# Performance work log

Measured on AMD Instinct MI355X. Metric: run time of the kernel, lower is better.

The kernel has to match this reference:

```python
import jax, jax.numpy as jnp
import numpy as np

N = 100000   # nodes
E = 1600000  # edges
G = 1024     # graphs
V = 51       # attr_dims[0]+1 embedding rows (padding_idx=0)
EMB = 32
H = 2        # heads
D = 64       # hidden_dim (per-head out channels)
DC = H * D   # 128 = dim_conv
NEG_GAT = 0.2   # PyG GATConv default negative_slope
NEG_ACT = 0.05  # module's leaky_relu slope
LN_EPS = 1e-5


def setup_inputs() -> dict:
    key = jax.random.key(0)
    ks = jax.random.split(key, 20)
    def nrm(k, shape, scale=0.1):
        return jax.random.normal(k, shape, dtype=jnp.float32) * scale
    x = jax.random.randint(ks[0], (N, 1), 0, V)
    edge_index = jax.random.randint(ks[1], (2, E), 0, N)
    batch_idx = jnp.sort(jax.random.randint(ks[2], (N,), 0, G))
    return {
        'x': x, 'edge_index': edge_index, 'batch_idx': batch_idx,
        'emb': nrm(ks[3], (V, EMB)).at[0].set(0.0),  # padding_idx=0
        'ln_g': jnp.ones((EMB,), jnp.float32), 'ln_b': jnp.zeros((EMB,), jnp.float32),
        'W1': nrm(ks[4], (EMB, DC)), 'a_src1': nrm(ks[5], (H, D)), 'a_dst1': nrm(ks[6], (H, D)), 'b1': nrm(ks[7], (DC,)),
        'W2': nrm(ks[8], (DC, DC)), 'a_src2': nrm(ks[9], (H, D)), 'a_dst2': nrm(ks[10], (H, D)), 'b2': nrm(ks[11], (DC,)),
        'gw1': nrm(ks[12], (DC, D)), 'gb1': nrm(ks[13], (D,)),
        'gw2': nrm(ks[14], (D, 1)), 'gb2': nrm(ks[15], (1,)),
    }


def _gat_conv(xf, src, dst, W, a_src, a_dst, b):
    # xf: [N, in]; returns [N, H*D]. PyG GATConv, eval mode (attn dropout off).
    xw = (xf @ W).reshape(N, H, D)                           # [N,H,D]
    al_s = jnp.einsum('nhd,hd->nh', xw, a_src)
    al_d = jnp.einsum('nhd,hd->nh', xw, a_dst)
    e = jax.nn.leaky_relu(al_s[src] + al_d[dst], NEG_GAT)    # [E',H]
    m = jax.ops.segment_max(e, dst, num_segments=N)
    ex = jnp.exp(e - m[dst])
    s = jax.ops.segment_sum(ex, dst, num_segments=N)
    alpha = ex / s[dst]                                      # segment softmax over incoming edges
    msg = xw[src] * alpha[:, :, None]                        # [E',H,D]
    out = jax.ops.segment_sum(msg, dst, num_segments=N)      # [N,H,D]
    return out.reshape(N, DC) + b


def reference(x, edge_index, batch_idx, emb, ln_g, ln_b,
              W1, a_src1, a_dst1, b1, W2, a_src2, a_dst2, b2,
              gw1, gb1, gw2, gb2):
    # embedding + LayerNorm (dropout off in eval)
    xe = emb[x[:, 0]]                                        # [N,32]
    mu = jnp.mean(xe, axis=-1, keepdims=True)
    var = jnp.var(xe, axis=-1, keepdims=True)
    xe = (xe - mu) * jax.lax.rsqrt(var + LN_EPS) * ln_g + ln_b
    # add self loops (GATConv add_self_loops=True)
    ar = jnp.arange(N, dtype=edge_index.dtype)
    src = jnp.concatenate([edge_index[0], ar])
    dst = jnp.concatenate([edge_index[1], ar])
    h = jax.nn.leaky_relu(_gat_conv(xe, src, dst, W1, a_src1, a_dst1, b1), NEG_ACT)
    h = _gat_conv(h, src, dst, W2, a_src2, a_dst2, b2)       # [N,128]
    # attentional aggregation over graphs
    gate = jax.nn.leaky_relu(h @ gw1 + gb1, NEG_ACT) @ gw2 + gb2   # [N,1]
    gm = jax.ops.segment_max(gate, batch_idx, num_segments=G)
    ge = jnp.exp(gate - gm[batch_idx])
    gs = jax.ops.segment_sum(ge, batch_idx, num_segments=G)
    w = ge / gs[batch_idx]
    z = jax.ops.segment_sum(w * h, batch_idx, num_segments=G)      # [G,128]
    return h, z
```

## Files before the change

### kernel.cpp

```cpp
#include <hip/hip_runtime.h>
#include <hip/hip_bf16.h>
#include <stdint.h>

typedef unsigned short u16;
typedef unsigned int   u32;
typedef __attribute__((ext_vector_type(8))) short bf16x8;
typedef __attribute__((ext_vector_type(4))) float f32x4;

#define NEG_GAT 0.2f
#define NEG_ACT 0.05f
#define LN_EPS  1e-5f
#define NPARAM  15

__device__ __forceinline__ float bf2f(u32 bits16){
  union { u32 u; float f; } v; v.u = bits16 << 16; return v.f;
}
__device__ __forceinline__ u16 f2bf(float f){
  union { float f; u32 u; } v; v.f = f;
  u32 u = v.u;
  u32 r = (u + 0x7fffu + ((u >> 16) & 1u)) >> 16;
  return (u16)r;
}
__device__ __forceinline__ float lrelu(float x, float s){ return fmaxf(x, s * x); }

__device__ __forceinline__ int geti(const int* __restrict__ p, int i, int enc){
  return p[enc ? (2 * i) : i];
}


struct CvtParams {
  const void* src[NPARAM];
  float*      dst[NPARAM];
  int         n[NPARAM];
};

#define MAXB  2048

__global__ void k_detect(const u32* __restrict__ ln_g_raw, const int* __restrict__ ei_raw,
                         int* __restrict__ flags, int* __restrict__ bcnt)
{
  const int t = threadIdx.x;
  for (int i = t; i < MAXB; i += 256) bcnt[i] = 0;
  if (t == 0){
    flags[0] = (ln_g_raw[0] == 0x3F800000u) ? 0 : 1;
    int zeros = 0;
    for (int j = 0; j < 64; j++) if (ei_raw[2 * j + 1] == 0) zeros++;
    flags[1] = (zeros >= 60) ? 1 : 0;
    flags[2] = 0;
    flags[3] = 0;
  }
}

__global__ void k_convert(CvtParams P, const int* __restrict__ flag)
{
  const int pi  = blockIdx.y;
  const int idx = blockIdx.x * 256 + threadIdx.x;
  if (idx >= P.n[pi]) return;
  if (*flag == 0) P.dst[pi][idx] = ((const float*)P.src[pi])[idx];
  else            P.dst[pi][idx] = bf2f(((const u16*)P.src[pi])[idx]);
}


__global__ void k_checks(const int* __restrict__ batch, const int* __restrict__ x,
                         const int* __restrict__ iflag,
                         int n, int V, int* __restrict__ errflag)
{
  int i = blockIdx.x * 256 + threadIdx.x;
  const int enc = *iflag;
  if (i < n){
    int v = geti(x, i, enc);
    if ((unsigned)v >= (unsigned)V) atomicOr(errflag, 16);
    if (i < n - 1 && geti(batch, i, enc) > geti(batch, i + 1, enc)) atomicOr(errflag, 8);
  }
}

__global__ void k_check_edges(const int* __restrict__ ei, const int* __restrict__ iflag,
                              int E, int n, int* __restrict__ errflag)
{
  int e = blockIdx.x * 256 + threadIdx.x;
  if (e < E){
    int enc = *iflag;
    int s = geti(ei, e, enc);
    int d = geti(ei, E + e, enc);
    if ((unsigned)s >= (unsigned)n || (unsigned)d >= (unsigned)n) atomicOr(errflag, 32);
  }
}


__global__ void k_hist(const int* __restrict__ ei, const int* __restrict__ iflag,
                       int* __restrict__ counts, int E, int n)
{
  int e = blockIdx.x * 256 + threadIdx.x;
  if (e < E){
    int d = geti(ei, E + e, *iflag);
    d = min(max(d, 0), n - 1);
    atomicAdd(&counts[d], 1);
  }
}

__global__ void k_scanA(const int* __restrict__ counts, int* __restrict__ rowptr,
                        int* __restrict__ bsums, int n)
{
  __shared__ int sd[1024];
  int tid = threadIdx.x;
  int gid = blockIdx.x * 1024 + tid;
  int v = (gid < n) ? counts[gid] : 0;
  sd[tid] = v;
  __syncthreads();
  for (int off = 1; off < 1024; off <<= 1){
    int t = 0;
    if (tid >= off) t = sd[tid - off];
    __syncthreads();
    if (tid >= off) sd[tid] += t;
    __syncthreads();
  }
  if (gid < n) rowptr[gid] = sd[tid] - v;
  if (tid == 1023) bsums[blockIdx.x] = sd[1023];
}

__global__ void k_scanB(const int* __restrict__ bsums, int* __restrict__ boffs, int nb)
{
  __shared__ int sd[128];
  int tid = threadIdx.x;
  int v = (tid < nb) ? bsums[tid] : 0;
  sd[tid] = v;
  __syncthreads();
  for (int off = 1; off < 128; off <<= 1){
    int t = 0;
    if (tid >= off) t = sd[tid - off];
    __syncthreads();
    if (tid >= off) sd[tid] += t;
    __syncthreads();
  }
  if (tid < nb) boffs[tid] = sd[tid] - v;
}

__global__ void k_scanC(int* __restrict__ rowptr, const int* __restrict__ boffs,
                        int* __restrict__ cursor, int n, int Etot)
{
  int gid = blockIdx.x * 1024 + threadIdx.x;
  if (gid < n){
    int v = rowptr[gid] + boffs[blockIdx.x];
    rowptr[gid] = v;
    cursor[gid] = v;
  }
  if (gid == 0) rowptr[n] = Etot;
}

__global__ void k_scatter(const int* __restrict__ ei, const int* __restrict__ iflag,
                          int* __restrict__ cursor, int* __restrict__ csr, int E, int n)
{
  int e = blockIdx.x * 256 + threadIdx.x;
  if (e < E){
    int enc = *iflag;
    int s = geti(ei, e, enc);
    int d = geti(ei, E + e, enc);
    d = min(max(d, 0), n - 1);
    int pos = atomicAdd(&cursor[d], 1);
    csr[pos] = s;
  }
}

__global__ void k_check_rows(const int* __restrict__ rowptr, const int* __restrict__ cursor,
                             int n, int* __restrict__ errflag)
{
  int i = blockIdx.x * 256 + threadIdx.x;
  if (i < n){
    if (cursor[i] != rowptr[i + 1]) atomicOr(errflag, 1);
    if (i == 0 && rowptr[0] != 0)   atomicOr(errflag, 4);
  }
}

__global__ void k_check_csr(const int* __restrict__ csr, int E, int n, int* __restrict__ errflag)
{
  int e = blockIdx.x * 256 + threadIdx.x;
  if (e < E && (unsigned)csr[e] >= (unsigned)n) atomicOr(errflag, 2);
}


#define BSH   9
#define BSZ   512
#define BMSK  511
#define BINB  8192
#define BTH   512

__global__ void k_bhist(const int* __restrict__ ei, const int* __restrict__ iflag,
                        int* __restrict__ bcnt, int E, int N, int nbuck)
{
  __shared__ int h[MAXB];
  const int t = threadIdx.x;
  for (int i = t; i < nbuck; i += 256) h[i] = 0;
  __syncthreads();
  const int enc = *iflag;
  for (int e = blockIdx.x * 256 + t; e < E; e += gridDim.x * 256){
    int d = geti(ei, E + e, enc);
    d = min(max(d, 0), N - 1);
    atomicAdd(&h[d >> BSH], 1);
  }
  __syncthreads();
  for (int i = t; i < nbuck; i += 256){
    int c = h[i];
    if (c) atomicAdd(&bcnt[i], c);
  }
}

__global__ void k_bscan(const int* __restrict__ bcnt, int* __restrict__ boff,
                        int* __restrict__ gcur, int* __restrict__ rowptr,
                        int nbuck, int N, int E)
{
  __shared__ int sd[MAXB];
  const int lane = threadIdx.x;
  for (int i = lane; i < nbuck; i += 64) sd[i] = bcnt[i];
  __syncthreads();
  const int L = (nbuck + 63) >> 6;
  const int b0 = lane * L;
  int sum = 0;
  for (int j = 0; j < L; j++){ int idx = b0 + j; if (idx < nbuck) sum += sd[idx]; }
  int excl = sum;
  for (int off = 1; off < 64; off <<= 1){
    int x = __shfl_up(excl, off);
    if (lane >= off) excl += x;
  }
  excl -= sum;
  int run = excl;
  for (int j = 0; j < L; j++){
    int idx = b0 + j;
    if (idx < nbuck){ boff[idx] = run; gcur[idx] = run; run += sd[idx]; }
  }
  if (lane == 0){ boff[nbuck] = E; rowptr[N] = E; }
}

__global__ __launch_bounds__(BTH) void k_bbin(
    const int* __restrict__ ei, const int* __restrict__ iflag,
    int* __restrict__ gcur, u32* __restrict__ binned,
    int E, int N, int nbuck, int* __restrict__ errflag)
{
  __shared__ u32 stage[BINB];
  __shared__ u16 sbk[BINB];
  __shared__ int hist[MAXB];
  __shared__ int base[MAXB];
  __shared__ int gpos[MAXB];
  const int t   = threadIdx.x;
  const int e0  = blockIdx.x * BINB;
  const int cnt = min(BINB, E - e0);
  const int enc = *iflag;

  for (int i = t; i < nbuck; i += BTH) hist[i] = 0;
  __syncthreads();

  u32 pv[16]; int bk[16]; int rk[16];
  int bad = 0;
  #pragma unroll
  for (int k = 0; k < 16; k++){
    bk[k] = -1;
    int lo = k * BTH + t;
    if (lo < cnt){
      int e = e0 + lo;
      int s = geti(ei, e, enc);
      int d = geti(ei, E + e, enc);
      if ((unsigned)s >= (unsigned)N || (unsigned)d >= (unsigned)N) bad = 1;
      s = min(max(s, 0), N - 1);
      d = min(max(d, 0), N - 1);
      int b = d >> BSH;
      pv[k] = ((u32)s << BSH) | (u32)(d & BMSK);
      bk[k] = b;
      rk[k] = atomicAdd(&hist[b], 1);
    }
  }
  if (bad) atomicOr(errflag, 32);
  __syncthreads();

  if (t < 64){
    const int L = (nbuck + 63) >> 6;
    const int b0 = t * L;
    int sum = 0;
    for (int j = 0; j < L; j++){ int idx = b0 + j; if (idx < nbuck) sum += hist[idx]; }
    int excl = sum;
    for (int off = 1; off < 64; off <<= 1){
      int x = __shfl_up(excl, off);
      if (t >= off) excl += x;
    }
    excl -= sum;
    int run = excl;
    for (int j = 0; j < L; j++){
      int idx = b0 + j;
      if (idx < nbuck){ base[idx] = run; run += hist[idx]; }
    }
  }
  __syncthreads();

  for (int i = t; i < nbuck; i += BTH){
    int c = hist[i];
    gpos[i] = c ? atomicAdd(&gcur[i], c) : 0;
  }
  __syncthreads();

  #pragma unroll
  for (int k = 0; k < 16; k++){
    if (bk[k] >= 0){
      int slot = base[bk[k]] + rk[k];
      stage[slot] = pv[k];
      sbk[slot]   = (u16)bk[k];
    }
  }
  __syncthreads();

  for (int j = t; j < cnt; j += BTH){
    int b = sbk[j];
    binned[gpos[b] + (j - base[b])] = stage[j];
  }
}

__global__ __launch_bounds__(256) void k_bcsr(
    const u32* __restrict__ binned, const int* __restrict__ boff,
    int* __restrict__ rowptr, int* __restrict__ csr, int N, int nbuck)
{
  __shared__ int cnt[BSZ];
  __shared__ int rp[BSZ];
  __shared__ int cur[BSZ];
  const int b = blockIdx.x;
  const int t = threadIdx.x;
  const int lo = boff[b], hi = boff[b + 1];

  for (int i = t; i < BSZ; i += 256){ cnt[i] = 0; cur[i] = 0; }
  __syncthreads();

  for (int j = lo + t; j < hi; j += 256)
    atomicAdd(&cnt[binned[j] & BMSK], 1);
  __syncthreads();

  if (t < 64){
    const int b0 = t * 8;
    int sum = 0;
    #pragma unroll
    for (int j = 0; j < 8; j++) sum += cnt[b0 + j];
    int excl = sum;
    for (int off = 1; off < 64; off <<= 1){
      int x = __shfl_up(excl, off);
      if (t >= off) excl += x;
    }
    excl -= sum;
    int run = excl;
    #pragma unroll
    for (int j = 0; j < 8; j++){ rp[b0 + j] = run; run += cnt[b0 + j]; }
  }
  __syncthreads();

  const int node0 = b << BSH;
  for (int i = t; i < BSZ; i += 256){
    int node = node0 + i;
    if (node < N) rowptr[node] = lo + rp[i];
  }

  for (int j = lo + t; j < hi; j += 256){
    u32 pvv = binned[j];
    int dl  = pvv & BMSK;
    int pos = lo + rp[dl] + atomicAdd(&cur[dl], 1);
    csr[pos] = (int)(pvv >> BSH);
  }
}


__global__ void k_stamp_if(const int* __restrict__ errflag, float* __restrict__ out, int nel)
{
  int f = *errflag;
  if (f == 0) return;
  float s = 500.0f + 100.0f * (float)f;
  for (int i = blockIdx.x * 256 + threadIdx.x; i < nel; i += gridDim.x * 256) out[i] = s;
}

__global__ void k_stamp(float* __restrict__ out, int nel, float val)
{
  for (int i = blockIdx.x * 256 + threadIdx.x; i < nel; i += gridDim.x * 256) out[i] = val;
}


__global__ __launch_bounds__(128) void k_tables(
    const float* __restrict__ emb,
    const float* __restrict__ ln_g, const float* __restrict__ ln_b,
    const float* __restrict__ W1, const float* __restrict__ a_src,
    const float* __restrict__ a_dst,
    const float* __restrict__ W2, const float* __restrict__ gw1,
    int V,
    u16* __restrict__ xwv, float* __restrict__ alsv, float* __restrict__ aldv,
    u16* __restrict__ pb2, u16* __restrict__ pbg)
{
  const int bid = blockIdx.x;
  const int t   = threadIdx.x;

  if (bid >= V){
    if (t >= 64) return;
    int pw = bid - V;
    const float* W; int ncols, ntiles, blk; u16* pb;
    if (pw < 32){ W = W2; ncols = 128; ntiles = 8; blk = pw;      pb = pb2; }
    else        { W = gw1; ncols = 64;  ntiles = 4; blk = pw - 32; pb = pbg; }
    const int ktile = blk / ntiles;
    const int ntile = blk % ntiles;
    const int n  = ntile * 16 + (t & 15);
    const int k0 = ktile * 32 + (t >> 4) * 8;
    u16* dst = pb + ((size_t)blk * 64 + t) * 8;
    #pragma unroll
    for (int j = 0; j < 8; j++)
      dst[j] = f2bf(W[(k0 + j) * ncols + n]);
    return;
  }

  __shared__ float se[32];
  __shared__ float stats[2];
  __shared__ float sxw[128];
  const int v = bid;
  if (t < 32) se[t] = emb[v * 32 + t];
  __syncthreads();
  if (t == 0){
    float s1 = 0.f, s2 = 0.f;
    for (int k = 0; k < 32; k++){ s1 += se[k]; s2 += se[k] * se[k]; }
    float mu = s1 * (1.f / 32.f);
    float var = s2 * (1.f / 32.f) - mu * mu;
    stats[0] = mu; stats[1] = rsqrtf(var + LN_EPS);
  }
  __syncthreads();
  const float mu = stats[0], rs = stats[1];
  float o = 0.f;
  for (int k = 0; k < 32; k++){
    float xe = (se[k] - mu) * rs * ln_g[k] + ln_b[k];
    o += xe * W1[k * 128 + t];
  }
  sxw[t] = o;
  xwv[v * 128 + t] = f2bf(o);
  __syncthreads();
  if (t < 2){
    float ps = 0.f, pd = 0.f;
    for (int d = 0; d < 64; d++){
      float vv = sxw[t * 64 + d];
      ps += vv * a_src[t * 64 + d];
      pd += vv * a_dst[t * 64 + d];
    }
    alsv[2 * v + t] = ps;
    aldv[2 * v + t] = pd;
  }
}


__global__ __launch_bounds__(256, 4) void k_gatw1(
    const int* __restrict__ rowptr, const int* __restrict__ csr,
    const int* __restrict__ x, const int* __restrict__ iflag,
    const float* __restrict__ alsv, const float* __restrict__ aldv,
    const u16* __restrict__ xwv, const float* __restrict__ bias,
    int N, int V, u16* __restrict__ out)
{
  extern __shared__ char smem[];
  float4* sedge = (float4*)smem;
  u16*    sxwv  = (u16*)(smem + 4096);
  float*  ET    = (float*)(smem + 4096 + (size_t)V * 256);

  const int tid = threadIdx.x;
  const int enc = *iflag;

  {
    const uint4* gx = (const uint4*)xwv;
    uint4* lx = (uint4*)sxwv;
    for (int idx = tid; idx < V * 16; idx += 256) lx[idx] = gx[idx];
  }
  {
    const int tot = V * V;
    for (int idx = tid; idx < tot; idx += 256){
      int vi = idx / V, v = idx - vi * V;
      ET[idx * 2]     = lrelu(alsv[2 * v]     + aldv[2 * vi],     NEG_GAT);
      ET[idx * 2 + 1] = lrelu(alsv[2 * v + 1] + aldv[2 * vi + 1], NEG_GAT);
    }
  }
  __syncthreads();
  {
    for (int r = tid; r < V * 2; r += 256){
      int vi = r >> 1, h = r & 1;
      float m = -3.0e38f;
      for (int v = 0; v < V; v++) m = fmaxf(m, ET[(vi * V + v) * 2 + h]);
      for (int v = 0; v < V; v++){
        int idx = (vi * V + v) * 2 + h;
        ET[idx] = __expf(ET[idx] - m);
      }
    }
  }
  __syncthreads();

  const int wave = tid >> 6;
  const int lane = tid & 63;
  const int sub  = lane >> 4;
  const int c16  = lane & 15;
  float4* mst = sedge + wave * 64;

  for (int i = blockIdx.x * 4 + wave; i < N; i += gridDim.x * 4){
    const int r0 = rowptr[i], deg = rowptr[i + 1] - r0, total = deg + 1;
    int vi = geti(x, i, enc); vi = min(max(vi, 0), V - 1);
    const float* ETrow = ET + (size_t)vi * V * 2;

    float sum0 = 0.f, sum1 = 0.f;
    float acc[8];
    #pragma unroll
    for (int r = 0; r < 8; r++) acc[r] = 0.f;

    for (int base = 0; base < total; base += 64){
      int k = base + lane;
      int vs = vi; float w0 = 0.f, w1 = 0.f;
      if (k < total){
        int s = (k < deg) ? csr[r0 + k] : i;
        int v = geti(x, s, enc);
        vs = min(max(v, 0), V - 1);
        float2 wv = *(const float2*)(ETrow + vs * 2);
        w0 = wv.x; w1 = wv.y;
      }
      sum0 += w0; sum1 += w1;
      mst[lane] = make_float4(__int_as_float(vs), w0, w1, 0.f);
      int cnt = min(64, total - base);
      int qmax = (cnt + 3) & ~3;
      for (int q = 0; q < qmax; q += 4){
        float4 md = mst[q + sub];
        int   vj = __float_as_int(md.x);
        float ej = (c16 < 8) ? md.y : md.z;
        uint4 w = *(const uint4*)(sxwv + vj * 128 + c16 * 8);
        acc[0] += ej * bf2f(w.x & 0xffffu); acc[1] += ej * bf2f(w.x >> 16);
        acc[2] += ej * bf2f(w.y & 0xffffu); acc[3] += ej * bf2f(w.y >> 16);
        acc[4] += ej * bf2f(w.z & 0xffffu); acc[5] += ej * bf2f(w.z >> 16);
        acc[6] += ej * bf2f(w.w & 0xffffu); acc[7] += ej * bf2f(w.w >> 16);
      }
    }

    #pragma unroll
    for (int off = 32; off; off >>= 1){
      sum0 += __shfl_xor(sum0, off);
      sum1 += __shfl_xor(sum1, off);
    }
    #pragma unroll
    for (int r = 0; r < 8; r++){
      acc[r] += __shfl_xor(acc[r], 16);
      acc[r] += __shfl_xor(acc[r], 32);
    }

    if (sub == 0){
      float inv = 1.f / ((c16 < 8) ? sum0 : sum1);
      const float4* bp = (const float4*)(bias + c16 * 8);
      float4 b0 = bp[0], b1 = bp[1];
      float o[8];
      o[0] = lrelu(acc[0] * inv + b0.x, NEG_ACT); o[1] = lrelu(acc[1] * inv + b0.y, NEG_ACT);
      o[2] = lrelu(acc[2] * inv + b0.z, NEG_ACT); o[3] = lrelu(acc[3] * inv + b0.w, NEG_ACT);
      o[4] = lrelu(acc[4] * inv + b1.x, NEG_ACT); o[5] = lrelu(acc[5] * inv + b1.y, NEG_ACT);
      o[6] = lrelu(acc[6] * inv + b1.z, NEG_ACT); o[7] = lrelu(acc[7] * inv + b1.w, NEG_ACT);
      uint4 pk;
      pk.x = (u32)f2bf(o[0]) | ((u32)f2bf(o[1]) << 16);
      pk.y = (u32)f2bf(o[2]) | ((u32)f2bf(o[3]) << 16);
      pk.z = (u32)f2bf(o[4]) | ((u32)f2bf(o[5]) << 16);
      pk.w = (u32)f2bf(o[6]) | ((u32)f2bf(o[7]) << 16);
      *(uint4*)(out + (size_t)i * 128 + c16 * 8) = pk;
    }
  }
}

__global__ __launch_bounds__(64, 8) void k_gatw1g(
    const int* __restrict__ rowptr, const int* __restrict__ csr,
    const int* __restrict__ x, const int* __restrict__ iflag,
    const float* __restrict__ alsv, const float* __restrict__ aldv,
    const u16* __restrict__ xwv, const float* __restrict__ bias,
    int V, u16* __restrict__ out)
{
  const int i    = blockIdx.x;
  const int lane = threadIdx.x;
  const int sub  = lane >> 4;
  const int c16  = lane & 15;
  const int enc  = *iflag;
  const int r0 = rowptr[i], deg = rowptr[i + 1] - r0, total = deg + 1;
  int vi = geti(x, i, enc); vi = min(max(vi, 0), V - 1);
  const float ad0 = aldv[2 * vi], ad1 = aldv[2 * vi + 1];

  float sum0 = 0.f, sum1 = 0.f;
  float acc[8];
  #pragma unroll
  for (int r = 0; r < 8; r++) acc[r] = 0.f;

  float m0 = -3.0e38f, m1 = -3.0e38f;
  for (int k = lane; k < total; k += 64){
    int s = (k < deg) ? csr[r0 + k] : i;
    int v = geti(x, s, enc); v = min(max(v, 0), V - 1);
    float2 as = *(const float2*)(alsv + 2 * v);
    m0 = fmaxf(m0, lrelu(as.x + ad0, NEG_GAT));
    m1 = fmaxf(m1, lrelu(as.y + ad1, NEG_GAT));
  }
  #pragma unroll
  for (int off = 32; off; off >>= 1){
    m0 = fmaxf(m0, __shfl_xor(m0, off));
    m1 = fmaxf(m1, __shfl_xor(m1, off));
  }
  for (int base = 0; base < total; base += 64){
    int k = base + lane;
    int vs = vi; float ex0 = 0.f, ex1 = 0.f;
    if (k < total){
      int s = (k < deg) ? csr[r0 + k] : i;
      int v = geti(x, s, enc); vs = min(max(v, 0), V - 1);
      float2 as = *(const float2*)(alsv + 2 * vs);
      ex0 = __expf(lrelu(as.x + ad0, NEG_GAT) - m0);
      ex1 = __expf(lrelu(as.y + ad1, NEG_GAT) - m1);
    }
    sum0 += ex0; sum1 += ex1;
    int cnt = min(64, total - base);
    int qmax = (cnt + 3) & ~3;
    for (int q = 0; q < qmax; q += 4){
      int   j  = q + sub;
      int   vj = __shfl(vs, j);
      float e0 = __shfl(ex0, j);
      float e1 = __shfl(ex1, j);
      float ej = (c16 < 8) ? e0 : e1;
      uint4 w = *(const uint4*)(xwv + (size_t)vj * 128 + c16 * 8);
      acc[0] += ej * bf2f(w.x & 0xffffu); acc[1] += ej * bf2f(w.x >> 16);
      acc[2] += ej * bf2f(w.y & 0xffffu); acc[3] += ej * bf2f(w.y >> 16);
      acc[4] += ej * bf2f(w.z & 0xffffu); acc[5] += ej * bf2f(w.z >> 16);
      acc[6] += ej * bf2f(w.w & 0xffffu); acc[7] += ej * bf2f(w.w >> 16);
    }
  }

  #pragma unroll
  for (int off = 32; off; off >>= 1){
    sum0 += __shfl_xor(sum0, off);
    sum1 += __shfl_xor(sum1, off);
  }
  #pragma unroll
  for (int r = 0; r < 8; r++){
    acc[r] += __shfl_xor(acc[r], 16);
    acc[r] += __shfl_xor(acc[r], 32);
  }

  if (sub == 0){
    float inv = 1.f / ((c16 < 8) ? sum0 : sum1);
    const float4* bp = (const float4*)(bias + c16 * 8);
    float4 b0 = bp[0], b1 = bp[1];
    float o[8];
    o[0] = lrelu(acc[0] * inv + b0.x, NEG_ACT); o[1] = lrelu(acc[1] * inv + b0.y, NEG_ACT);
    o[2] = lrelu(acc[2] * inv + b0.z, NEG_ACT); o[3] = lrelu(acc[3] * inv + b0.w, NEG_ACT);
    o[4] = lrelu(acc[4] * inv + b1.x, NEG_ACT); o[5] = lrelu(acc[5] * inv + b1.y, NEG_ACT);
    o[6] = lrelu(acc[6] * inv + b1.z, NEG_ACT); o[7] = lrelu(acc[7] * inv + b1.w, NEG_ACT);
    uint4 pk;
    pk.x = (u32)f2bf(o[0]) | ((u32)f2bf(o[1]) << 16);
    pk.y = (u32)f2bf(o[2]) | ((u32)f2bf(o[3]) << 16);
    pk.z = (u32)f2bf(o[4]) | ((u32)f2bf(o[5]) << 16);
    pk.w = (u32)f2bf(o[6]) | ((u32)f2bf(o[7]) << 16);
    *(uint4*)(out + (size_t)i * 128 + c16 * 8) = pk;
  }
}


__global__ __launch_bounds__(64, 8) void k_gatw2(
    const int* __restrict__ rowptr, const int* __restrict__ csr,
    const float* __restrict__ al_s, const float* __restrict__ al_d,
    const u16* __restrict__ xw, const float* __restrict__ bias,
    int apply_act, float* __restrict__ out)
{
  const int i    = blockIdx.x;
  const int lane = threadIdx.x;
  const int sub  = lane >> 4;
  const int c16  = lane & 15;
  const int r0 = rowptr[i], deg = rowptr[i + 1] - r0, total = deg + 1;
  const float2 ad = *(const float2*)(al_d + 2 * i);

  float sum0 = 0.f, sum1 = 0.f;
  float acc[8];
  #pragma unroll
  for (int r = 0; r < 8; r++) acc[r] = 0.f;

  if (total <= 64){
    int s = i;
    float a0 = -3.0e38f, a1 = -3.0e38f;
    if (lane < total){
      s = (lane < deg) ? csr[r0 + lane] : i;
      float2 as = *(const float2*)(al_s + 2 * s);
      a0 = lrelu(as.x + ad.x, NEG_GAT);
      a1 = lrelu(as.y + ad.y, NEG_GAT);
    }
    float m0 = a0, m1 = a1;
    #pragma unroll
    for (int off = 32; off; off >>= 1){
      m0 = fmaxf(m0, __shfl_xor(m0, off));
      m1 = fmaxf(m1, __shfl_xor(m1, off));
    }
    float ex0 = 0.f, ex1 = 0.f;
    if (lane < total){ ex0 = __expf(a0 - m0); ex1 = __expf(a1 - m1); }
    sum0 = ex0; sum1 = ex1;
    int qmax = (total + 3) & ~3;
    for (int q = 0; q < qmax; q += 4){
      int   j  = q + sub;
      int   sj = __shfl(s, j);
      float e0 = __shfl(ex0, j);
      float e1 = __shfl(ex1, j);
      float ej = (c16 < 8) ? e0 : e1;
      uint4 w = *(const uint4*)(xw + (size_t)sj * 128 + c16 * 8);
      acc[0] += ej * bf2f(w.x & 0xffffu); acc[1] += ej * bf2f(w.x >> 16);
      acc[2] += ej * bf2f(w.y & 0xffffu); acc[3] += ej * bf2f(w.y >> 16);
      acc[4] += ej * bf2f(w.z & 0xffffu); acc[5] += ej * bf2f(w.z >> 16);
      acc[6] += ej * bf2f(w.w & 0xffffu); acc[7] += ej * bf2f(w.w >> 16);
    }
  } else {
    float m0 = -3.0e38f, m1 = -3.0e38f;
    for (int k = lane; k < total; k += 64){
      int s = (k < deg) ? csr[r0 + k] : i;
      float2 as = *(const float2*)(al_s + 2 * s);
      m0 = fmaxf(m0, lrelu(as.x + ad.x, NEG_GAT));
      m1 = fmaxf(m1, lrelu(as.y + ad.y, NEG_GAT));
    }
    #pragma unroll
    for (int off = 32; off; off >>= 1){
      m0 = fmaxf(m0, __shfl_xor(m0, off));
      m1 = fmaxf(m1, __shfl_xor(m1, off));
    }
    for (int base = 0; base < total; base += 64){
      int k = base + lane;
      int s = i; float ex0 = 0.f, ex1 = 0.f;
      if (k < total){
        s = (k < deg) ? csr[r0 + k] : i;
        float2 as = *(const float2*)(al_s + 2 * s);
        ex0 = __expf(lrelu(as.x + ad.x, NEG_GAT) - m0);
        ex1 = __expf(lrelu(as.y + ad.y, NEG_GAT) - m1);
      }
      sum0 += ex0; sum1 += ex1;
      int cnt = min(64, total - base);
      int qmax = (cnt + 3) & ~3;
      for (int q = 0; q < qmax; q += 4){
        int   j  = q + sub;
        int   sj = __shfl(s, j);
        float e0 = __shfl(ex0, j);
        float e1 = __shfl(ex1, j);
        float ej = (c16 < 8) ? e0 : e1;
        uint4 w = *(const uint4*)(xw + (size_t)sj * 128 + c16 * 8);
        acc[0] += ej * bf2f(w.x & 0xffffu); acc[1] += ej * bf2f(w.x >> 16);
        acc[2] += ej * bf2f(w.y & 0xffffu); acc[3] += ej * bf2f(w.y >> 16);
        acc[4] += ej * bf2f(w.z & 0xffffu); acc[5] += ej * bf2f(w.z >> 16);
        acc[6] += ej * bf2f(w.w & 0xffffu); acc[7] += ej * bf2f(w.w >> 16);
      }
    }
  }

  #pragma unroll
  for (int off = 32; off; off >>= 1){
    sum0 += __shfl_xor(sum0, off);
    sum1 += __shfl_xor(sum1, off);
  }
  #pragma unroll
  for (int r = 0; r < 8; r++){
    acc[r] += __shfl_xor(acc[r], 16);
    acc[r] += __shfl_xor(acc[r], 32);
  }

  if (sub == 0){
    float inv = 1.f / ((c16 < 8) ? sum0 : sum1);
    const float4* bp = (const float4*)(bias + c16 * 8);
    float4 b0 = bp[0], b1 = bp[1];
    float4 o0, o1;
    o0.x = acc[0] * inv + b0.x; o0.y = acc[1] * inv + b0.y;
    o0.z = acc[2] * inv + b0.z; o0.w = acc[3] * inv + b0.w;
    o1.x = acc[4] * inv + b1.x; o1.y = acc[5] * inv + b1.y;
    o1.z = acc[6] * inv + b1.z; o1.w = acc[7] * inv + b1.w;
    if (apply_act){
      o0.x = lrelu(o0.x, NEG_ACT); o0.y = lrelu(o0.y, NEG_ACT);
      o0.z = lrelu(o0.z, NEG_ACT); o0.w = lrelu(o0.w, NEG_ACT);
      o1.x = lrelu(o1.x, NEG_ACT); o1.y = lrelu(o1.y, NEG_ACT);
      o1.z = lrelu(o1.z, NEG_ACT); o1.w = lrelu(o1.w, NEG_ACT);
    }
    float* op = out + (size_t)i * 128 + c16 * 8;
    *(float4*)op       = o0;
    *(float4*)(op + 4) = o1;
  }
}


__global__ __launch_bounds__(256, 2) void k_node2m(
    const u16* __restrict__ h1b, const u16* __restrict__ pb2,
    const float* __restrict__ a_src, const float* __restrict__ a_dst,
    int N, u16* __restrict__ xw, float* __restrict__ al_s, float* __restrict__ al_d)
{
  const int wave = threadIdx.x >> 6;
  const int lane = threadIdx.x & 63;
  const int rowbase = blockIdx.x * 64 + wave * 16;
  const int m    = lane & 15;
  const int quad = lane >> 4;

  int arow = rowbase + m; if (arow >= N) arow = N - 1;
  const u16* aptr = h1b + (size_t)arow * 128 + quad * 8;

  f32x4 acc[8];
  #pragma unroll
  for (int nt = 0; nt < 8; nt++) acc[nt] = (f32x4){0.f, 0.f, 0.f, 0.f};

  #pragma unroll
  for (int kt = 0; kt < 4; kt++){
    bf16x8 af = *(const bf16x8*)(aptr + kt * 32);
    const u16* bbase = pb2 + (((size_t)kt * 8) * 64 + lane) * 8;
    #pragma unroll
    for (int nt = 0; nt < 8; nt++){
      bf16x8 bf = *(const bf16x8*)(bbase + (size_t)nt * 64 * 8);
      acc[nt] = __builtin_amdgcn_mfma_f32_16x16x32_bf16(af, bf, acc[nt], 0, 0, 0);
    }
  }

  float asv[8], adv[8];
  #pragma unroll
  for (int nt = 0; nt < 8; nt++){
    asv[nt] = a_src[nt * 16 + m];
    adv[nt] = a_dst[nt * 16 + m];
  }
  #pragma unroll
  for (int r = 0; r < 4; r++){
    int row = rowbase + quad * 4 + r;
    bool ok = row < N;
    float s0 = 0.f, s1 = 0.f, d0 = 0.f, d1 = 0.f;
    #pragma unroll
    for (int nt = 0; nt < 8; nt++){
      float v = acc[nt][r];
      if (ok) xw[(size_t)row * 128 + nt * 16 + m] = f2bf(v);
      if (nt < 4){ s0 += v * asv[nt]; d0 += v * adv[nt]; }
      else       { s1 += v * asv[nt]; d1 += v * adv[nt]; }
    }
    #pragma unroll
    for (int off = 1; off < 16; off <<= 1){
      s0 += __shfl_xor(s0, off); s1 += __shfl_xor(s1, off);
      d0 += __shfl_xor(d0, off); d1 += __shfl_xor(d1, off);
    }
    if (ok && m == 0){
      al_s[2 * row] = s0; al_s[2 * row + 1] = s1;
      al_d[2 * row] = d0; al_d[2 * row + 1] = d1;
    }
  }
}


__global__ __launch_bounds__(256, 2) void k_gatem(
    const float* __restrict__ h, const u16* __restrict__ pbg,
    const float* __restrict__ gb1, const float* __restrict__ gw2,
    const float* __restrict__ gb2, int N, float* __restrict__ gate)
{
  const int wave = threadIdx.x >> 6;
  const int lane = threadIdx.x & 63;
  const int rowbase = blockIdx.x * 64 + wave * 16;
  const int m    = lane & 15;
  const int quad = lane >> 4;

  int arow = rowbase + m; if (arow >= N) arow = N - 1;
  const float* aptr = h + (size_t)arow * 128 + quad * 8;

  f32x4 acc[4];
  #pragma unroll
  for (int nt = 0; nt < 4; nt++) acc[nt] = (f32x4){0.f, 0.f, 0.f, 0.f};

  #pragma unroll
  for (int kt = 0; kt < 4; kt++){
    float4 a0 = *(const float4*)(aptr + kt * 32);
    float4 a1 = *(const float4*)(aptr + kt * 32 + 4);
    bf16x8 af;
    af[0] = (short)f2bf(a0.x); af[1] = (short)f2bf(a0.y);
    af[2] = (short)f2bf(a0.z); af[3] = (short)f2bf(a0.w);
    af[4] = (short)f2bf(a1.x); af[5] = (short)f2bf(a1.y);
    af[6] = (short)f2bf(a1.z); af[7] = (short)f2bf(a1.w);
    const u16* bbase = pbg + (((size_t)kt * 4) * 64 + lane) * 8;
    #pragma unroll
    for (int nt = 0; nt < 4; nt++){
      bf16x8 bf = *(const bf16x8*)(bbase + (size_t)nt * 64 * 8);
      acc[nt] = __builtin_amdgcn_mfma_f32_16x16x32_bf16(af, bf, acc[nt], 0, 0, 0);
    }
  }

  float gbv[4], g2v[4];
  #pragma unroll
  for (int nt = 0; nt < 4; nt++){
    gbv[nt] = gb1[nt * 16 + m];
    g2v[nt] = gw2[nt * 16 + m];
  }
  const float g2b = gb2[0];
  #pragma unroll
  for (int r = 0; r < 4; r++){
    int row = rowbase + quad * 4 + r;
    float q = 0.f;
    #pragma unroll
    for (int nt = 0; nt < 4; nt++)
      q += lrelu(acc[nt][r] + gbv[nt], NEG_ACT) * g2v[nt];
    #pragma unroll
    for (int off = 1; off < 16; off <<= 1) q += __shfl_xor(q, off);
    if (row < N && m == 0) gate[row] = q + g2b;
  }
}


__global__ __launch_bounds__(512) void k_graphsw(
    const int* __restrict__ batch, const int* __restrict__ iflag,
    const float* __restrict__ gate,
    const float* __restrict__ h, float* __restrict__ zout, int N)
{
  __shared__ int   range[2];
  __shared__ float red[16];
  __shared__ float sz[3][128];
  const int g = blockIdx.x, t = threadIdx.x;
  const int wave = t >> 6, lane = t & 63;
  if (t == 0){
    const int enc = *iflag;
    int lo = 0, hi = N;
    while (lo < hi){ int mid = (lo + hi) >> 1; if (geti(batch, mid, enc) < g) lo = mid + 1; else hi = mid; }
    range[0] = lo;
    hi = N;
    while (lo < hi){ int mid = (lo + hi) >> 1; if (geti(batch, mid, enc) < g + 1) lo = mid + 1; else hi = mid; }
    range[1] = lo;
  }
  __syncthreads();
  const int st = range[0], en = range[1];

  float m = -3.0e38f;
  for (int k = st + t; k < en; k += 512) m = fmaxf(m, gate[k]);
  #pragma unroll
  for (int off = 32; off; off >>= 1) m = fmaxf(m, __shfl_xor(m, off));
  if (lane == 0) red[wave] = m;
  __syncthreads();
  m = red[0];
  #pragma unroll
  for (int w = 1; w < 8; w++) m = fmaxf(m, red[w]);

  float s = 0.f;
  for (int k = st + t; k < en; k += 512) s += __expf(gate[k] - m);
  #pragma unroll
  for (int off = 32; off; off >>= 1) s += __shfl_xor(s, off);
  if (lane == 0) red[8 + wave] = s;
  __syncthreads();
  s = red[8];
  #pragma unroll
  for (int w = 9; w < 16; w++) s += red[w];

  const float inv = 1.f / s;
  const int quarter = t >> 7, t2 = t & 127;
  float z = 0.f;
  for (int k = st + quarter; k < en; k += 4){
    float wk = __expf(gate[k] - m) * inv;
    z += wk * h[(size_t)k * 128 + t2];
  }
  if (quarter) sz[quarter - 1][t2] = z;
  __syncthreads();
  if (quarter == 0) zout[(size_t)g * 128 + t2] = z + sz[0][t2] + sz[1][t2] + sz[2][t2];
}


extern "C" void kernel_launch(void* const* d_in, const int* in_sizes, int n_in,
                              void* d_out, int out_size, void* d_ws, size_t ws_size,
                              hipStream_t stream)
{
  const int* x      = (const int*)d_in[0];
  const int* ei     = (const int*)d_in[1];
  const int* batch  = (const int*)d_in[2];

  const int N = in_sizes[0];
  const int E = in_sizes[1] / 2;
  const int V = in_sizes[3] / 32;
  const int G = out_size / 128 - N;

  char* p = (char*)d_ws;
  auto alloc = [&](size_t bytes) -> char* {
    char* r = p; p += (bytes + 255) & ~(size_t)255; return r;
  };
  int*   multi  = (int*)  alloc((size_t)N * 4);
  int*   rowptr = (int*)  alloc((size_t)(N + 1) * 4);
  int*   csr    = (int*)  alloc((size_t)E * 4);
  int*   bsums  = (int*)  alloc(4096);
  int*   boffs  = (int*)  alloc(4096);
  int*   flags  = (int*)  alloc(256);
  int*   fflag  = flags;
  int*   iflag  = flags + 1;
  int*   errflg = flags + 2;
  float* al_s   = (float*)alloc((size_t)N * 2 * 4);
  float* al_d   = (float*)alloc((size_t)N * 2 * 4);
  u16*   xw     = (u16*)  alloc((size_t)N * 128 * 2);
  u16*   h1b    = (u16*)  alloc((size_t)N * 128 * 2);
  u16*   xwv    = (u16*)  alloc((size_t)V * 128 * 2);
  float* alsv   = (float*)alloc((size_t)V * 2 * 4);
  float* aldv   = (float*)alloc((size_t)V * 2 * 4);
  u16*   pb2    = (u16*)  alloc((size_t)128 * 128 * 2);
  u16*   pbg    = (u16*)  alloc((size_t)128 * 64 * 2);

  const int nbuck = (N + BSZ - 1) >> BSH;
  int*   bcnt   = (int*)  alloc((size_t)(MAXB) * 4);
  int*   boff   = (int*)  alloc((size_t)(MAXB + 1) * 4);
  int*   gcur   = (int*)  alloc((size_t)(MAXB) * 4);
  u32*   binned = (u32*)  alloc((size_t)E * 4);

  CvtParams cp;
  float* fpar[NPARAM];
  int maxn = 0;
  for (int pi = 0; pi < NPARAM; pi++){
    int n = in_sizes[3 + pi];
    fpar[pi] = (float*)alloc((size_t)n * 4);
    cp.src[pi] = d_in[3 + pi];
    cp.dst[pi] = fpar[pi];
    cp.n[pi]   = n;
    if (n > maxn) maxn = n;
  }
  const size_t needed = (size_t)(p - (char*)d_ws);

  const float* emb    = fpar[0];
  const float* ln_g   = fpar[1];
  const float* ln_b   = fpar[2];
  const float* W1     = fpar[3];
  const float* a_src1 = fpar[4];
  const float* a_dst1 = fpar[5];
  const float* b1     = fpar[6];
  const float* W2     = fpar[7];
  const float* a_src2 = fpar[8];
  const float* a_dst2 = fpar[9];
  const float* b2     = fpar[10];
  const float* gw1    = fpar[11];
  const float* gb1    = fpar[12];
  const float* gw2    = fpar[13];
  const float* gb2    = fpar[14];
  (void)n_in;

  if (ws_size < needed){
    k_stamp<<<512, 256, 0, stream>>>((float*)d_out, out_size, 9999.0f);
    return;
  }

  int*   counts = multi;
  int*   cursor = multi;
  float* gate   = (float*)multi;
  float* hbuf   = (float*)d_out;
  float* zbuf   = (float*)d_out + (size_t)N * 128;

  k_detect<<<1, 256, 0, stream>>>((const u32*)d_in[4], ei, flags, bcnt);
  dim3 cgrid((maxn + 255) / 256, NPARAM);
  k_convert<<<cgrid, 256, 0, stream>>>(cp, fflag);

  int eb = (E + 255) / 256;
  int nb = (N + 1023) / 1024;
  int nb256 = (N + 255) / 256;

  k_checks<<<nb256, 256, 0, stream>>>(batch, x, iflag, N, V, errflg);

  if (nbuck <= MAXB){
    k_bhist<<<256, 256, 0, stream>>>(ei, iflag, bcnt, E, N, nbuck);
    k_bscan<<<1, 64, 0, stream>>>(bcnt, boff, gcur, rowptr, nbuck, N, E);
    k_bbin<<<(E + BINB - 1) / BINB, BTH, 0, stream>>>(ei, iflag, gcur, binned, E, N, nbuck, errflg);
    k_bcsr<<<nbuck, 256, 0, stream>>>(binned, boff, rowptr, csr, N, nbuck);
  } else {
    k_check_edges<<<eb, 256, 0, stream>>>(ei, iflag, E, N, errflg);
    hipMemsetAsync(counts, 0, (size_t)N * 4, stream);
    hipMemsetAsync(csr, 0xFF, (size_t)E * 4, stream);
    k_hist<<<eb, 256, 0, stream>>>(ei, iflag, counts, E, N);
    k_scanA<<<nb, 1024, 0, stream>>>(counts, rowptr, bsums, N);
    k_scanB<<<1, 128, 0, stream>>>(bsums, boffs, nb);
    k_scanC<<<nb, 1024, 0, stream>>>(rowptr, boffs, cursor, N, E);
    k_scatter<<<eb, 256, 0, stream>>>(ei, iflag, cursor, csr, E, N);
    k_check_rows<<<nb256, 256, 0, stream>>>(rowptr, cursor, N, errflg);
    k_check_csr<<<eb, 256, 0, stream>>>(csr, E, N, errflg);
  }

  k_tables<<<V + 48, 128, 0, stream>>>(emb, ln_g, ln_b, W1, a_src1, a_dst1,
                                       W2, gw1, V, xwv, alsv, aldv, pb2, pbg);

  const size_t smem1 = 4096 + (size_t)V * 256 + (size_t)V * V * 8;
  if (V <= 64 && smem1 <= 64 * 1024){
    const int gwb = min(1024, (N + 3) / 4);
    k_gatw1<<<gwb, 256, smem1, stream>>>(rowptr, csr, x, iflag, alsv, aldv, xwv, b1, N, V, h1b);
  } else {
    k_gatw1g<<<N, 64, 0, stream>>>(rowptr, csr, x, iflag, alsv, aldv, xwv, b1, V, h1b);
  }

  const int gblk = (N + 63) / 64;
  k_node2m<<<gblk, 256, 0, stream>>>(h1b, pb2, a_src2, a_dst2, N, xw, al_s, al_d);

  k_gatw2<<<N, 64, 0, stream>>>(rowptr, csr, al_s, al_d, xw, b2, 0, hbuf);

  k_gatem<<<gblk, 256, 0, stream>>>(hbuf, pbg, gb1, gw2, gb2, N, gate);
  k_graphsw<<<G, 512, 0, stream>>>(batch, iflag, gate, hbuf, zbuf, N);

  k_stamp_if<<<512, 256, 0, stream>>>(errflg, (float*)d_out, out_size);
}
```

Baseline: 353.2 us.

## Fuse gate MLP into graph pooling kernel and fold input checks into CSR build

Removes the separate MFMA gate kernel and computes the gate scores inside the per-graph pooling kernel with an fp32 scalar dot product against gw1 held in shared memory. Each block handles one graph, so the rows of h it reads for the gate are read again right after for pooling. The x and batch validity checks move from their own kernel into k_bcsr, which cuts two launches. In exchange, the gate matmul drops from tensor-core MFMA to scalar FMA over LDS, and each block's 32KB+ of shared memory may limit occupancy.

```diff
diff --git a/kernel.cpp b/kernel.cpp
--- a/kernel.cpp
+++ b/kernel.cpp
@@ -313,7 +313,10 @@
 
 __global__ __launch_bounds__(256) void k_bcsr(
     const u32* __restrict__ binned, const int* __restrict__ boff,
-    int* __restrict__ rowptr, int* __restrict__ csr, int N, int nbuck)
+    const int* __restrict__ x, const int* __restrict__ batch,
+    const int* __restrict__ iflag, int V,
+    int* __restrict__ rowptr, int* __restrict__ csr, int N, int nbuck,
+    int* __restrict__ errflag)
 {
   __shared__ int cnt[BSZ];
   __shared__ int rp[BSZ];
@@ -321,8 +324,20 @@
   const int b = blockIdx.x;
   const int t = threadIdx.x;
   const int lo = boff[b], hi = boff[b + 1];
+  const int enc = *iflag;
+  const int node0 = b << BSH;
 
   for (int i = t; i < BSZ; i += 256){ cnt[i] = 0; cur[i] = 0; }
+
+  for (int i = t; i < BSZ; i += 256){
+    int node = node0 + i;
+    if (node < N){
+      int v = geti(x, node, enc);
+      if ((unsigned)v >= (unsigned)V) atomicOr(errflag, 16);
+      if (node < N - 1 && geti(batch, node, enc) > geti(batch, node + 1, enc))
+        atomicOr(errflag, 8);
+    }
+  }
   __syncthreads();
 
   for (int j = lo + t; j < hi; j += 256)
@@ -336,8 +351,8 @@
     for (int j = 0; j < 8; j++) sum += cnt[b0 + j];
     int excl = sum;
     for (int off = 1; off < 64; off <<= 1){
-      int x = __shfl_up(excl, off);
-      if (t >= off) excl += x;
+      int xq = __shfl_up(excl, off);
+      if (t >= off) excl += xq;
     }
     excl -= sum;
     int run = excl;
@@ -346,7 +361,6 @@
   }
   __syncthreads();
 
-  const int node0 = b << BSH;
   for (int i = t; i < BSZ; i += 256){
     int node = node0 + i;
     if (node < N) rowptr[node] = lo + rp[i];
@@ -380,28 +394,25 @@
     const float* __restrict__ ln_g, const float* __restrict__ ln_b,
     const float* __restrict__ W1, const float* __restrict__ a_src,
     const float* __restrict__ a_dst,
-    const float* __restrict__ W2, const float* __restrict__ gw1,
+    const float* __restrict__ W2,
     int V,
     u16* __restrict__ xwv, float* __restrict__ alsv, float* __restrict__ aldv,
-    u16* __restrict__ pb2, u16* __restrict__ pbg)
+    u16* __restrict__ pb2)
 {
   const int bid = blockIdx.x;
   const int t   = threadIdx.x;
 
   if (bid >= V){
     if (t >= 64) return;
-    int pw = bid - V;
-    const float* W; int ncols, ntiles, blk; u16* pb;
-    if (pw < 32){ W = W2; ncols = 128; ntiles = 8; blk = pw;      pb = pb2; }
-    else        { W = gw1; ncols = 64;  ntiles = 4; blk = pw - 32; pb = pbg; }
-    const int ktile = blk / ntiles;
-    const int ntile = blk % ntiles;
+    int blk = bid - V;
+    const int ktile = blk / 8;
+    const int ntile = blk % 8;
     const int n  = ntile * 16 + (t & 15);
     const int k0 = ktile * 32 + (t >> 4) * 8;
-    u16* dst = pb + ((size_t)blk * 64 + t) * 8;
+    u16* dst = pb2 + ((size_t)blk * 64 + t) * 8;
     #pragma unroll
     for (int j = 0; j < 8; j++)
-      dst[j] = f2bf(W[(k0 + j) * ncols + n]);
+      dst[j] = f2bf(W2[(k0 + j) * 128 + n]);
     return;
   }
 
@@ -828,70 +839,18 @@
 }
 
 
-__global__ __launch_bounds__(256, 2) void k_gatem(
-    const float* __restrict__ h, const u16* __restrict__ pbg,
-    const float* __restrict__ gb1, const float* __restrict__ gw2,
-    const float* __restrict__ gb2, int N, float* __restrict__ gate)
-{
-  const int wave = threadIdx.x >> 6;
-  const int lane = threadIdx.x & 63;
-  const int rowbase = blockIdx.x * 64 + wave * 16;
-  const int m    = lane & 15;
-  const int quad = lane >> 4;
-
-  int arow = rowbase + m; if (arow >= N) arow = N - 1;
-  const float* aptr = h + (size_t)arow * 128 + quad * 8;
-
-  f32x4 acc[4];
-  #pragma unroll
-  for (int nt = 0; nt < 4; nt++) acc[nt] = (f32x4){0.f, 0.f, 0.f, 0.f};
-
-  #pragma unroll
-  for (int kt = 0; kt < 4; kt++){
-    float4 a0 = *(const float4*)(aptr + kt * 32);
-    float4 a1 = *(const float4*)(aptr + kt * 32 + 4);
-    bf16x8 af;
-    af[0] = (short)f2bf(a0.x); af[1] = (short)f2bf(a0.y);
-    af[2] = (short)f2bf(a0.z); af[3] = (short)f2bf(a0.w);
-    af[4] = (short)f2bf(a1.x); af[5] = (short)f2bf(a1.y);
-    af[6] = (short)f2bf(a1.z); af[7] = (short)f2bf(a1.w);
-    const u16* bbase = pbg + (((size_t)kt * 4) * 64 + lane) * 8;
-    #pragma unroll
-    for (int nt = 0; nt < 4; nt++){
-      bf16x8 bf = *(const bf16x8*)(bbase + (size_t)nt * 64 * 8);
-      acc[nt] = __builtin_amdgcn_mfma_f32_16x16x32_bf16(af, bf, acc[nt], 0, 0, 0);
-    }
-  }
-
-  float gbv[4], g2v[4];
-  #pragma unroll
-  for (int nt = 0; nt < 4; nt++){
-    gbv[nt] = gb1[nt * 16 + m];
-    g2v[nt] = gw2[nt * 16 + m];
-  }
-  const float g2b = gb2[0];
-  #pragma unroll
-  for (int r = 0; r < 4; r++){
-    int row = rowbase + quad * 4 + r;
-    float q = 0.f;
-    #pragma unroll
-    for (int nt = 0; nt < 4; nt++)
-      q += lrelu(acc[nt][r] + gbv[nt], NEG_ACT) * g2v[nt];
-    #pragma unroll
-    for (int off = 1; off < 16; off <<= 1) q += __shfl_xor(q, off);
-    if (row < N && m == 0) gate[row] = q + g2b;
-  }
-}
-
-
-__global__ __launch_bounds__(512) void k_graphsw(
+__global__ __launch_bounds__(512) void k_gatepool(
     const int* __restrict__ batch, const int* __restrict__ iflag,
-    const float* __restrict__ gate,
+    const float* __restrict__ gw1, const float* __restrict__ gb1,
+    const float* __restrict__ gw2, const float* __restrict__ gb2,
+    float* __restrict__ gate,
     const float* __restrict__ h, float* __restrict__ zout, int N)
 {
   __shared__ int   range[2];
   __shared__ float red[16];
   __shared__ float sz[3][128];
+  __shared__ float gwl[128 * 64];
+  __shared__ float sh[8][128];
   const int g = blockIdx.x, t = threadIdx.x;
   const int wave = t >> 6, lane = t & 63;
   if (t == 0){
@@ -903,8 +862,28 @@
     while (lo < hi){ int mid = (lo + hi) >> 1; if (geti(batch, mid, enc) < g + 1) lo = mid + 1; else hi = mid; }
     range[1] = lo;
   }
+  for (int idx = t; idx < 128 * 64; idx += 512) gwl[idx] = gw1[idx];
   __syncthreads();
   const int st = range[0], en = range[1];
+
+  {
+    const float g1b = gb1[lane];
+    const float g2w = gw2[lane];
+    const float g2b = gb2[0];
+    for (int k = st + wave; k < en; k += 8){
+      float2 hv = *(const float2*)(h + (size_t)k * 128 + lane * 2);
+      sh[wave][lane * 2]     = hv.x;
+      sh[wave][lane * 2 + 1] = hv.y;
+      float td = 0.f;
+      #pragma unroll 8
+      for (int j = 0; j < 128; j++) td += sh[wave][j] * gwl[j * 64 + lane];
+      float q = lrelu(td + g1b, NEG_ACT) * g2w;
+      #pragma unroll
+      for (int off = 32; off; off >>= 1) q += __shfl_xor(q, off);
+      if (lane == 0) gate[k] = q + g2b;
+    }
+  }
+  __syncthreads();
 
   float m = -3.0e38f;
   for (int k = st + t; k < en; k += 512) m = fmaxf(m, gate[k]);
@@ -973,7 +952,6 @@
   float* alsv   = (float*)alloc((size_t)V * 2 * 4);
   float* aldv   = (float*)alloc((size_t)V * 2 * 4);
   u16*   pb2    = (u16*)  alloc((size_t)128 * 128 * 2);
-  u16*   pbg    = (u16*)  alloc((size_t)128 * 64 * 2);
 
   const int nbuck = (N + BSZ - 1) >> BSH;
   int*   bcnt   = (int*)  alloc((size_t)(MAXB) * 4);
@@ -1030,14 +1008,13 @@
   int nb = (N + 1023) / 1024;
   int nb256 = (N + 255) / 256;
 
-  k_checks<<<nb256, 256, 0, stream>>>(batch, x, iflag, N, V, errflg);
-
   if (nbuck <= MAXB){
     k_bhist<<<256, 256, 0, stream>>>(ei, iflag, bcnt, E, N, nbuck);
     k_bscan<<<1, 64, 0, stream>>>(bcnt, boff, gcur, rowptr, nbuck, N, E);
     k_bbin<<<(E + BINB - 1) / BINB, BTH, 0, stream>>>(ei, iflag, gcur, binned, E, N, nbuck, errflg);
-    k_bcsr<<<nbuck, 256, 0, stream>>>(binned, boff, rowptr, csr, N, nbuck);
+    k_bcsr<<<nbuck, 256, 0, stream>>>(binned, boff, x, batch, iflag, V, rowptr, csr, N, nbuck, errflg);
   } else {
+    k_checks<<<nb256, 256, 0, stream>>>(batch, x, iflag, N, V, errflg);
     k_check_edges<<<eb, 256, 0, stream>>>(ei, iflag, E, N, errflg);
     hipMemsetAsync(counts, 0, (size_t)N * 4, stream);
     hipMemsetAsync(csr, 0xFF, (size_t)E * 4, stream);
@@ -1050,8 +1027,8 @@
     k_check_csr<<<eb, 256, 0, stream>>>(csr, E, N, errflg);
   }
 
-  k_tables<<<V + 48, 128, 0, stream>>>(emb, ln_g, ln_b, W1, a_src1, a_dst1,
-                                       W2, gw1, V, xwv, alsv, aldv, pb2, pbg);
+  k_tables<<<V + 32, 128, 0, stream>>>(emb, ln_g, ln_b, W1, a_src1, a_dst1,
+                                       W2, V, xwv, alsv, aldv, pb2);
 
   const size_t smem1 = 4096 + (size_t)V * 256 + (size_t)V * V * 8;
   if (V <= 64 && smem1 <= 64 * 1024){
@@ -1066,8 +1043,7 @@
 
   k_gatw2<<<N, 64, 0, stream>>>(rowptr, csr, al_s, al_d, xw, b2, 0, hbuf);
 
-  k_gatem<<<gblk, 256, 0, stream>>>(hbuf, pbg, gb1, gw2, gb2, N, gate);
-  k_graphsw<<<G, 512, 0, stream>>>(batch, iflag, gate, hbuf, zbuf, N);
+  k_gatepool<<<G, 512, 0, stream>>>(batch, iflag, gw1, gb1, gw2, gb2, gate, hbuf, zbuf, N);
 
   k_stamp_if<<<512, 256, 0, stream>>>(errflg, (float*)d_out, out_size);
 }
```

After: 430.0 us. 21.7% more time.
